# Kernel optimization log

Hardware: AMD Instinct MI355X
Metric: run time of the kernel (lower is better)

## Reference

```python
import jax, jax.numpy as jnp
import numpy as np

B, N, D, K = 32, 4096, 128, 512
NPB = 2048          # unique tail nodes per batch (>= K so topk branch is taken)
M = B * NPB         # total unique tail nodes
E = B * N           # total edges
NUM_ENT = 10000


def setup_inputs() -> dict:
    key = jax.random.key(0)
    ks = jax.random.split(key, 18)
    f = lambda k, s: jax.random.normal(k, s, dtype=jnp.float32)
    inp = {
        "q_head": f(ks[0], (B, D)),
        "q_rel": f(ks[1], (B, D)),
        "q_time": f(ks[2], (B, D)),
        "r_neighbor": f(ks[3], (B, N, D)),
        "t_neighbor": f(ks[4], (B, N, D)),
        "time_neighbor": f(ks[5], (B, N, D)),
        "hidden": f(ks[6], (E, D)),
        "tail_emd": jnp.zeros((M, D), jnp.float32),  # scatter out-buffer
    }
    # tail_index: each edge of batch b scatters into that batch's node slab
    local = jax.random.randint(ks[7], (B, N), 0, NPB)
    inp["tail_index"] = (local + jnp.arange(B)[:, None] * NPB).reshape(E).astype(jnp.int32)
    # tail_nodes: [M,3] = (batch id, tail entity, time)
    batch_col = jnp.repeat(jnp.arange(B), NPB)
    tail_col = jax.random.randint(ks[8], (M,), 0, NUM_ENT)
    time_col = jax.random.randint(ks[9], (M,), 0, 365)
    inp["tail_nodes"] = jnp.stack([batch_col, tail_col, time_col], axis=-1).astype(jnp.int32)
    # linear-layer params (torch nn.Linear-style scaling)
    s3, s1 = 1.0 / np.sqrt(3 * D), 1.0 / np.sqrt(D)
    inp["W_q"] = f(ks[10], (3 * D, D)) * s3
    inp["b_q"] = jnp.zeros((D,), jnp.float32)
    inp["W_a"] = f(ks[11], (3 * D, D)) * s3
    inp["b_a"] = jnp.zeros((D,), jnp.float32)
    inp["W_att"] = f(ks[12], (3 * D, 1)) * s3
    inp["b_att"] = jnp.zeros((1,), jnp.float32)
    inp["W_rule"] = f(ks[13], (D, 1)) * s1
    inp["b_rule"] = jnp.zeros((1,), jnp.float32)
    inp["W_out"] = f(ks[14], (D, D)) * s1
    inp["b_out"] = jnp.zeros((D,), jnp.float32)
    return inp


def reference(q_head, q_rel, q_time, r_neighbor, t_neighbor, time_neighbor,
              hidden, tail_emd, tail_index, tail_nodes,
              W_q, b_q, W_a, b_a, W_att, b_att, W_rule, b_rule, W_out, b_out):
    # act = identity (module default). reduce = 'sum'.
    # raw message per edge: [E, D]
    message = (q_head[:, None, :] + r_neighbor + time_neighbor).reshape(E, D)
    # query / neighbor projections
    query = jnp.concatenate([q_head, q_rel, q_time], axis=-1) @ W_q + b_q      # [B, D]
    neigh = jnp.concatenate([r_neighbor, t_neighbor, time_neighbor], -1) @ W_a + b_a  # [B, N, D]
    q = query[:, None, :]
    qa = jnp.concatenate([q * neigh, q - neigh, q + neigh], axis=-1)           # [B, N, 3D]
    att1 = jax.nn.sigmoid(qa @ W_att + b_att).reshape(E, 1)
    att2 = jax.nn.sigmoid(hidden @ W_rule + b_rule)                            # [E, 1]
    att = (att1 + att2) * 0.5
    msg = att * message
    # scatter-sum aggregation over unique tail nodes
    seg = lambda v: jax.ops.segment_sum(v, tail_index, num_segments=M)
    tail_agg = tail_emd + seg(msg)            # scatter(..., out=tail_emd)
    new_hidden = seg(hidden)                  # [M, D]
    agg_att = seg(att[:, 0])                  # [M]
    # per-batch top-k over aggregated attention (each batch has NPB >= K nodes)
    nodes_batch = tail_nodes[:, 0]
    scores = jnp.where(nodes_batch[None, :] == jnp.arange(B)[:, None],
                       agg_att[None, :], -jnp.inf)                             # [B, M]
    _, idx = jax.lax.top_k(scores, K)                                          # [B, K] global node ids
    new_nodes = jnp.stack([tail_nodes[:, 1][idx], tail_nodes[:, 2][idx]], -1)  # [B, K, 2]
    emd = tail_agg[idx]                                                        # [B, K, D]
    hid = new_hidden[idx]                                                      # [B, K, D]
    out_emd = emd @ W_out + b_out                                              # act=identity
    return new_nodes, out_emd, hid
```

## Files before the change

### kernel.cpp

```cpp
#include <hip/hip_runtime.h>
#include <math.h>

#define B 32
#define N 4096
#define D 128
#define KTOP 512
#define NPB 2048
#define MSEG (B * NPB)
#define E (B * N)
#define MAXC 32
#define K7ROWS 16

__global__ __launch_bounds__(384) void k0_precompute(
    const float* __restrict__ qh, const float* __restrict__ qr,
    const float* __restrict__ qt, const float* __restrict__ Wq,
    const float* __restrict__ bq, const float* __restrict__ Wa,
    const float* __restrict__ ba, const float* __restrict__ Watt,
    const float* __restrict__ batt, float* __restrict__ vf,
    float* __restrict__ c2f, int* __restrict__ counts,
    double* __restrict__ aggd) {
  int b = blockIdx.x;
  int tid = threadIdx.x;
  {
    int t = b * 384 + tid;
    float4 z = make_float4(0.f, 0.f, 0.f, 0.f);
    float4* cz = (float4*)counts;
    float4* az = (float4*)aggd;
    for (int i = t; i < 16384; i += 12288) cz[i] = z;
    for (int i = t; i < 32768; i += 12288) az[i] = z;
  }
  int d = tid & 127;
  int g = tid >> 7;
  __shared__ double part[3][128];
  __shared__ double u[128];
  __shared__ double red[128];
  const float* xs = (g == 0 ? qh : (g == 1 ? qr : qt)) + b * 128;
  const float* Wg = Wq + g * 128 * 128;
  double a0 = 0, a1 = 0, a2 = 0, a3 = 0;
#pragma unroll 4
  for (int i = 0; i < 128; i += 4) {
    a0 += (double)xs[i] * (double)Wg[i * 128 + d];
    a1 += (double)xs[i + 1] * (double)Wg[(i + 1) * 128 + d];
    a2 += (double)xs[i + 2] * (double)Wg[(i + 2) * 128 + d];
    a3 += (double)xs[i + 3] * (double)Wg[(i + 3) * 128 + d];
  }
  part[g][d] = (a0 + a1) + (a2 + a3);
  __syncthreads();
  if (g == 0) {
    double acc = (double)bq[d] + part[0][d] + part[1][d] + part[2][d];
    double w1 = (double)Watt[d], w2 = (double)Watt[128 + d],
           w3 = (double)Watt[256 + d];
    double ud = acc * w1 - w2 + w3;
    u[d] = ud;
    red[d] = acc * (w2 + w3) + (double)ba[d] * ud;
  }
  __syncthreads();
  for (int s = 64; s > 0; s >>= 1) {
    if (tid < s) red[tid] += red[tid + s];
    __syncthreads();
  }
  if (tid == 0) c2f[b] = (float)(red[0] + (double)batt[0]);
  {
    double v0 = 0, v1 = 0, v2 = 0, v3 = 0;
    const float* Wr = Wa + tid * 128;
#pragma unroll 4
    for (int dd = 0; dd < 128; dd += 4) {
      v0 += (double)Wr[dd] * u[dd];
      v1 += (double)Wr[dd + 1] * u[dd + 1];
      v2 += (double)Wr[dd + 2] * u[dd + 2];
      v3 += (double)Wr[dd + 3] * u[dd + 3];
    }
    vf[b * 384 + tid] = (float)((v0 + v1) + (v2 + v3));
  }
}

__global__ __launch_bounds__(256, 8) void k1_att(
    const float* __restrict__ r, const float* __restrict__ t,
    const float* __restrict__ tm, const float* __restrict__ hidden,
    const float* __restrict__ Wrule, const float* __restrict__ brule,
    const float* __restrict__ vf, const float* __restrict__ c2f,
    const int* __restrict__ tidx, float* __restrict__ attw,
    double* __restrict__ aggd, int* __restrict__ counts,
    int* __restrict__ lists) {
  int tid = threadIdx.x;
  int h = tid >> 5;
  int l = tid & 31;
  int base = blockIdx.x * 64;
  int b = base >> 12;
  const float4* vb = (const float4*)(vf + b * 384);
  float4 v0 = vb[l];
  float4 v1 = vb[32 + l];
  float4 v2 = vb[64 + l];
  float4 wr = ((const float4*)Wrule)[l];
  float c2 = c2f[b];
  float br = brule[0];
  int myseg = 0;
  if (l < 8) myseg = tidx[base + l * 8 + h];
  float mya = 0.f;
  unsigned lo = (unsigned)(l * 4);
  float4 ra[2], ta[2], ma[2], ha[2];
  {
    unsigned eo = ((unsigned)(base + h) << 7) + lo;
    ra[0] = *(const float4*)(r + eo);
    ta[0] = *(const float4*)(t + eo);
    ma[0] = *(const float4*)(tm + eo);
    ha[0] = *(const float4*)(hidden + eo);
  }
#pragma unroll
  for (int i = 0; i < 8; ++i) {
    const int cur = i & 1;
    if (i < 7) {
      const int nxt = cur ^ 1;
      unsigned eo = ((unsigned)(base + (i + 1) * 8 + h) << 7) + lo;
      ra[nxt] = *(const float4*)(r + eo);
      ta[nxt] = *(const float4*)(t + eo);
      ma[nxt] = *(const float4*)(tm + eo);
      ha[nxt] = *(const float4*)(hidden + eo);
    }
    float4 A = ra[cur], T = ta[cur], M = ma[cur], H = ha[cur];
    float p1 = A.x * v0.x + A.y * v0.y + A.z * v0.z + A.w * v0.w;
    p1 += T.x * v1.x + T.y * v1.y + T.z * v1.z + T.w * v1.w;
    p1 += M.x * v2.x + M.y * v2.y + M.z * v2.z + M.w * v2.w;
    float p2 = H.x * wr.x + H.y * wr.y + H.z * wr.z + H.w * wr.w;
#pragma unroll
    for (int off = 16; off > 0; off >>= 1) {
      p1 += __shfl_xor(p1, off);
      p2 += __shfl_xor(p2, off);
    }
    if (l == i) {
      float a1 = 1.0f / (1.0f + expf(-(p1 + c2)));
      float a2 = 1.0f / (1.0f + expf(-(p2 + br)));
      mya = 0.5f * (a1 + a2);
    }
  }
  if (l < 8) {
    int e = base + l * 8 + h;
    attw[e] = mya;
    atomicAdd(&aggd[myseg], (double)mya);
    int pos = atomicAdd(&counts[myseg], 1);
    if (pos < MAXC) lists[myseg * MAXC + pos] = e;
  }
}

__global__ __launch_bounds__(256) void k6_topk(
    const double* __restrict__ aggd, const int* __restrict__ tail_nodes,
    float* __restrict__ out_nodes, int* __restrict__ idxw) {
  __shared__ double sv[2048];
  int b = blockIdx.x >> 3;
  int chunk = blockIdx.x & 7;
  int tid = threadIdx.x;
  for (int s = tid; s < 2048; s += 256) sv[s] = aggd[b * 2048 + s];
  __syncthreads();
  int i = chunk * 256 + tid;
  double vi = sv[i];
  int rank = 0;
#pragma unroll 8
  for (int j = 0; j < 2048; ++j) {
    double vj = sv[j];
    rank += (vj > vi) || (vj == vi && j < i);
  }
  if (rank < KTOP) {
    int gm = b * 2048 + i;
    int p = b * KTOP + rank;
    out_nodes[p * 2 + 0] = (float)tail_nodes[gm * 3 + 1];
    out_nodes[p * 2 + 1] = (float)tail_nodes[gm * 3 + 2];
    idxw[p] = gm;
  }
}

__global__ __launch_bounds__(256) void k7_out(
    const float* __restrict__ tail_emd, const float* __restrict__ r,
    const float* __restrict__ tm, const float* __restrict__ hidden,
    const float* __restrict__ qh, const float* __restrict__ attw,
    const int* __restrict__ counts, const int* __restrict__ lists,
    const float* __restrict__ Wout, const float* __restrict__ bout,
    const int* __restrict__ idxw, float* __restrict__ out_emd,
    float* __restrict__ out_hid) {
  __shared__ float es[K7ROWS][128];
  int tid = threadIdx.x;
  int sub = tid >> 7, d = tid & 127;
  int base = blockIdx.x * K7ROWS;
  int mrow[8], crow[8];
#pragma unroll
  for (int jj = 0; jj < 8; ++jj) mrow[jj] = idxw[base + jj * 2 + sub];
#pragma unroll
  for (int jj = 0; jj < 8; ++jj) crow[jj] = counts[mrow[jj]];
  int4 el[8];
#pragma unroll
  for (int jj = 0; jj < 8; ++jj)
    el[jj] = *(const int4*)(lists + (size_t)mrow[jj] * MAXC);
#pragma unroll
  for (int jj = 0; jj < 8; ++jj) {
    int m = mrow[jj];
    int bb = m >> 11;
    int cnt = crow[jj] > MAXC ? MAXC : crow[jj];
    float accT = tail_emd[(size_t)m * 128 + d];
    float accH = 0.f;
    float qhd = qh[bb * 128 + d];
    int e0 = el[jj].x, e1 = el[jj].y, e2 = el[jj].z, e3 = el[jj].w;
    if (cnt > 0) {
      float a = attw[e0];
      size_t eo = (size_t)e0 * 128 + d;
      accT += a * (qhd + r[eo] + tm[eo]);
      accH += hidden[eo];
    }
    if (cnt > 1) {
      float a = attw[e1];
      size_t eo = (size_t)e1 * 128 + d;
      accT += a * (qhd + r[eo] + tm[eo]);
      accH += hidden[eo];
    }
    if (cnt > 2) {
      float a = attw[e2];
      size_t eo = (size_t)e2 * 128 + d;
      accT += a * (qhd + r[eo] + tm[eo]);
      accH += hidden[eo];
    }
    if (cnt > 3) {
      float a = attw[e3];
      size_t eo = (size_t)e3 * 128 + d;
      accT += a * (qhd + r[eo] + tm[eo]);
      accH += hidden[eo];
    }
    for (int k = 4; k < cnt; ++k) {
      int e = lists[(size_t)m * MAXC + k];
      float a = attw[e];
      size_t eo = (size_t)e * 128 + d;
      accT += a * (qhd + r[eo] + tm[eo]);
      accH += hidden[eo];
    }
    es[jj * 2 + sub][d] = accT;
    out_hid[(size_t)(base + jj * 2 + sub) * 128 + d] = accH;
  }
  __syncthreads();
  int cg = tid & 31;
  int rg = tid >> 5;
  float4 bo = *(const float4*)(bout + cg * 4);
  float acc0x = bo.x, acc0y = bo.y, acc0z = bo.z, acc0w = bo.w;
  float acc1x = bo.x, acc1y = bo.y, acc1z = bo.z, acc1w = bo.w;
#pragma unroll 4
  for (int i = 0; i < 128; ++i) {
    float4 w = *(const float4*)(Wout + i * 128 + cg * 4);
    float e0 = es[rg * 2 + 0][i];
    float e1 = es[rg * 2 + 1][i];
    acc0x += e0 * w.x; acc0y += e0 * w.y; acc0z += e0 * w.z; acc0w += e0 * w.w;
    acc1x += e1 * w.x; acc1y += e1 * w.y; acc1z += e1 * w.z; acc1w += e1 * w.w;
  }
  size_t r0 = (size_t)(base + rg * 2) * 128 + cg * 4;
  *(float4*)(out_emd + r0) = make_float4(acc0x, acc0y, acc0z, acc0w);
  *(float4*)(out_emd + r0 + 128) = make_float4(acc1x, acc1y, acc1z, acc1w);
}

extern "C" void kernel_launch(void* const* d_in, const int* in_sizes, int n_in,
                              void* d_out, int out_size, void* d_ws,
                              size_t ws_size, hipStream_t stream) {
  const float* q_head = (const float*)d_in[0];
  const float* q_rel = (const float*)d_in[1];
  const float* q_time = (const float*)d_in[2];
  const float* r_nb = (const float*)d_in[3];
  const float* t_nb = (const float*)d_in[4];
  const float* tm_nb = (const float*)d_in[5];
  const float* hidden = (const float*)d_in[6];
  const float* tail_emd = (const float*)d_in[7];
  const int* tail_index = (const int*)d_in[8];
  const int* tail_nodes = (const int*)d_in[9];
  const float* W_q = (const float*)d_in[10];
  const float* b_q = (const float*)d_in[11];
  const float* W_a = (const float*)d_in[12];
  const float* b_a = (const float*)d_in[13];
  const float* W_att = (const float*)d_in[14];
  const float* b_att = (const float*)d_in[15];
  const float* W_rule = (const float*)d_in[16];
  const float* b_rule = (const float*)d_in[17];
  const float* W_out = (const float*)d_in[18];
  const float* b_out = (const float*)d_in[19];

  char* ws = (char*)d_ws;
  float* vf = (float*)(ws + 0);
  float* c2f = (float*)(ws + 49152);
  float* attw = (float*)(ws + 49280);
  int* counts = (int*)(ws + 573568);
  double* aggd = (double*)(ws + 835712);
  int* lists = (int*)(ws + 1360000);
  int* idxw = (int*)(ws + 9748608);

  float* out_nodes = (float*)d_out;
  float* out_emd = (float*)d_out + (size_t)B * KTOP * 2;
  float* out_hid = out_emd + (size_t)B * KTOP * 128;

  k0_precompute<<<B, 384, 0, stream>>>(q_head, q_rel, q_time, W_q, b_q, W_a,
                                       b_a, W_att, b_att, vf, c2f, counts,
                                       aggd);
  k1_att<<<E / 64, 256, 0, stream>>>(r_nb, t_nb, tm_nb, hidden, W_rule, b_rule,
                                     vf, c2f, tail_index, attw, aggd, counts,
                                     lists);
  k6_topk<<<B * 8, 256, 0, stream>>>(aggd, tail_nodes, out_nodes, idxw);
  k7_out<<<(B * KTOP) / K7ROWS, 256, 0, stream>>>(tail_emd, r_nb, tm_nb,
                                                  hidden, q_head, attw, counts,
                                                  lists, W_out, b_out, idxw,
                                                  out_emd, out_hid);
}
```

Measured before the change: 431.7 us.

## Store edge lists as 16-bit local ids, batch gather loads, halve k1 grid

Edge lists per segment now hold 16-bit batch-local edge ids instead of 32-bit global ids. This halves list storage and the first-entry load in the output kernel, which moves from an int4 to a uint2. The first four gathers in k7 are issued unconditionally and masked by multiplication rather than branches, so the loads can be in flight at the same time. k1 now processes two 64-edge chunks per block with half the grid, cutting per-block setup. The unconditional loads read garbage list slots when the count is below four. They stay in bounds only because the ids are masked into the batch range, and a garbage attw value that is NaN or Inf times a zero mask would give NaN.

```diff
diff --git a/kernel.cpp b/kernel.cpp
--- a/kernel.cpp
+++ b/kernel.cpp
@@ -81,12 +81,12 @@
     const float* __restrict__ vf, const float* __restrict__ c2f,
     const int* __restrict__ tidx, float* __restrict__ attw,
     double* __restrict__ aggd, int* __restrict__ counts,
-    int* __restrict__ lists) {
+    unsigned short* __restrict__ lists) {
   int tid = threadIdx.x;
   int h = tid >> 5;
   int l = tid & 31;
-  int base = blockIdx.x * 64;
-  int b = base >> 12;
+  int blk = blockIdx.x;
+  int b = blk >> 5;
   const float4* vb = (const float4*)(vf + b * 384);
   float4 v0 = vb[l];
   float4 v1 = vb[32 + l];
@@ -94,51 +94,55 @@
   float4 wr = ((const float4*)Wrule)[l];
   float c2 = c2f[b];
   float br = brule[0];
-  int myseg = 0;
-  if (l < 8) myseg = tidx[base + l * 8 + h];
-  float mya = 0.f;
   unsigned lo = (unsigned)(l * 4);
-  float4 ra[2], ta[2], ma[2], ha[2];
-  {
-    unsigned eo = ((unsigned)(base + h) << 7) + lo;
-    ra[0] = *(const float4*)(r + eo);
-    ta[0] = *(const float4*)(t + eo);
-    ma[0] = *(const float4*)(tm + eo);
-    ha[0] = *(const float4*)(hidden + eo);
-  }
-#pragma unroll
-  for (int i = 0; i < 8; ++i) {
-    const int cur = i & 1;
-    if (i < 7) {
-      const int nxt = cur ^ 1;
-      unsigned eo = ((unsigned)(base + (i + 1) * 8 + h) << 7) + lo;
-      ra[nxt] = *(const float4*)(r + eo);
-      ta[nxt] = *(const float4*)(t + eo);
-      ma[nxt] = *(const float4*)(tm + eo);
-      ha[nxt] = *(const float4*)(hidden + eo);
-    }
-    float4 A = ra[cur], T = ta[cur], M = ma[cur], H = ha[cur];
-    float p1 = A.x * v0.x + A.y * v0.y + A.z * v0.z + A.w * v0.w;
-    p1 += T.x * v1.x + T.y * v1.y + T.z * v1.z + T.w * v1.w;
-    p1 += M.x * v2.x + M.y * v2.y + M.z * v2.z + M.w * v2.w;
-    float p2 = H.x * wr.x + H.y * wr.y + H.z * wr.z + H.w * wr.w;
-#pragma unroll
-    for (int off = 16; off > 0; off >>= 1) {
-      p1 += __shfl_xor(p1, off);
-      p2 += __shfl_xor(p2, off);
-    }
-    if (l == i) {
-      float a1 = 1.0f / (1.0f + expf(-(p1 + c2)));
-      float a2 = 1.0f / (1.0f + expf(-(p2 + br)));
-      mya = 0.5f * (a1 + a2);
-    }
-  }
-  if (l < 8) {
-    int e = base + l * 8 + h;
-    attw[e] = mya;
-    atomicAdd(&aggd[myseg], (double)mya);
-    int pos = atomicAdd(&counts[myseg], 1);
-    if (pos < MAXC) lists[myseg * MAXC + pos] = e;
+  for (int pass = 0; pass < 2; ++pass) {
+    int base = blk * 128 + pass * 64;
+    int myseg = 0;
+    if (l < 8) myseg = tidx[base + l * 8 + h];
+    float mya = 0.f;
+    float4 ra[2], ta[2], ma[2], ha[2];
+    {
+      unsigned eo = ((unsigned)(base + h) << 7) + lo;
+      ra[0] = *(const float4*)(r + eo);
+      ta[0] = *(const float4*)(t + eo);
+      ma[0] = *(const float4*)(tm + eo);
+      ha[0] = *(const float4*)(hidden + eo);
+    }
+#pragma unroll
+    for (int i = 0; i < 8; ++i) {
+      const int cur = i & 1;
+      if (i < 7) {
+        const int nxt = cur ^ 1;
+        unsigned eo = ((unsigned)(base + (i + 1) * 8 + h) << 7) + lo;
+        ra[nxt] = *(const float4*)(r + eo);
+        ta[nxt] = *(const float4*)(t + eo);
+        ma[nxt] = *(const float4*)(tm + eo);
+        ha[nxt] = *(const float4*)(hidden + eo);
+      }
+      float4 A = ra[cur], T = ta[cur], M = ma[cur], H = ha[cur];
+      float p1 = A.x * v0.x + A.y * v0.y + A.z * v0.z + A.w * v0.w;
+      p1 += T.x * v1.x + T.y * v1.y + T.z * v1.z + T.w * v1.w;
+      p1 += M.x * v2.x + M.y * v2.y + M.z * v2.z + M.w * v2.w;
+      float p2 = H.x * wr.x + H.y * wr.y + H.z * wr.z + H.w * wr.w;
+#pragma unroll
+      for (int off = 16; off > 0; off >>= 1) {
+        p1 += __shfl_xor(p1, off);
+        p2 += __shfl_xor(p2, off);
+      }
+      if (l == i) {
+        float a1 = 1.0f / (1.0f + expf(-(p1 + c2)));
+        float a2 = 1.0f / (1.0f + expf(-(p2 + br)));
+        mya = 0.5f * (a1 + a2);
+      }
+    }
+    if (l < 8) {
+      int e = base + l * 8 + h;
+      attw[e] = mya;
+      atomicAdd(&aggd[myseg], (double)mya);
+      int pos = atomicAdd(&counts[myseg], 1);
+      if (pos < MAXC)
+        lists[(unsigned)myseg * MAXC + pos] = (unsigned short)(e & 4095);
+    }
   }
 }
 
@@ -172,7 +176,7 @@
     const float* __restrict__ tail_emd, const float* __restrict__ r,
     const float* __restrict__ tm, const float* __restrict__ hidden,
     const float* __restrict__ qh, const float* __restrict__ attw,
-    const int* __restrict__ counts, const int* __restrict__ lists,
+    const int* __restrict__ counts, const unsigned short* __restrict__ lists,
     const float* __restrict__ Wout, const float* __restrict__ bout,
     const int* __restrict__ idxw, float* __restrict__ out_emd,
     float* __restrict__ out_hid) {
@@ -185,47 +189,42 @@
   for (int jj = 0; jj < 8; ++jj) mrow[jj] = idxw[base + jj * 2 + sub];
 #pragma unroll
   for (int jj = 0; jj < 8; ++jj) crow[jj] = counts[mrow[jj]];
-  int4 el[8];
+  uint2 el[8];
 #pragma unroll
   for (int jj = 0; jj < 8; ++jj)
-    el[jj] = *(const int4*)(lists + (size_t)mrow[jj] * MAXC);
+    el[jj] = *(const uint2*)(lists + (size_t)mrow[jj] * MAXC);
 #pragma unroll
   for (int jj = 0; jj < 8; ++jj) {
     int m = mrow[jj];
     int bb = m >> 11;
+    unsigned ebase = (unsigned)bb << 12;
     int cnt = crow[jj] > MAXC ? MAXC : crow[jj];
     float accT = tail_emd[(size_t)m * 128 + d];
     float accH = 0.f;
     float qhd = qh[bb * 128 + d];
-    int e0 = el[jj].x, e1 = el[jj].y, e2 = el[jj].z, e3 = el[jj].w;
-    if (cnt > 0) {
-      float a = attw[e0];
-      size_t eo = (size_t)e0 * 128 + d;
-      accT += a * (qhd + r[eo] + tm[eo]);
-      accH += hidden[eo];
-    }
-    if (cnt > 1) {
-      float a = attw[e1];
-      size_t eo = (size_t)e1 * 128 + d;
-      accT += a * (qhd + r[eo] + tm[eo]);
-      accH += hidden[eo];
-    }
-    if (cnt > 2) {
-      float a = attw[e2];
-      size_t eo = (size_t)e2 * 128 + d;
-      accT += a * (qhd + r[eo] + tm[eo]);
-      accH += hidden[eo];
-    }
-    if (cnt > 3) {
-      float a = attw[e3];
-      size_t eo = (size_t)e3 * 128 + d;
-      accT += a * (qhd + r[eo] + tm[eo]);
-      accH += hidden[eo];
-    }
+    unsigned e0 = ebase | (el[jj].x & 0xFFFFu);
+    unsigned e1 = ebase | (el[jj].x >> 16);
+    unsigned e2 = ebase | (el[jj].y & 0xFFFFu);
+    unsigned e3 = ebase | (el[jj].y >> 16);
+    float m0 = cnt > 0 ? 1.f : 0.f;
+    float m1 = cnt > 1 ? 1.f : 0.f;
+    float m2 = cnt > 2 ? 1.f : 0.f;
+    float m3 = cnt > 3 ? 1.f : 0.f;
+    float a0 = attw[e0], a1 = attw[e1], a2 = attw[e2], a3 = attw[e3];
+    unsigned o0 = (e0 << 7) + d, o1 = (e1 << 7) + d;
+    unsigned o2 = (e2 << 7) + d, o3 = (e3 << 7) + d;
+    float r0 = r[o0], r1 = r[o1], r2 = r[o2], r3 = r[o3];
+    float t0 = tm[o0], t1 = tm[o1], t2 = tm[o2], t3 = tm[o3];
+    float h0 = hidden[o0], h1 = hidden[o1], h2 = hidden[o2], h3 = hidden[o3];
+    accT += m0 * a0 * (qhd + r0 + t0);
+    accT += m1 * a1 * (qhd + r1 + t1);
+    accT += m2 * a2 * (qhd + r2 + t2);
+    accT += m3 * a3 * (qhd + r3 + t3);
+    accH += m0 * h0 + m1 * h1 + m2 * h2 + m3 * h3;
     for (int k = 4; k < cnt; ++k) {
-      int e = lists[(size_t)m * MAXC + k];
+      unsigned e = ebase | lists[(size_t)m * MAXC + k];
       float a = attw[e];
-      size_t eo = (size_t)e * 128 + d;
+      unsigned eo = (e << 7) + d;
       accT += a * (qhd + r[eo] + tm[eo]);
       accH += hidden[eo];
     }
@@ -246,9 +245,9 @@
     acc0x += e0 * w.x; acc0y += e0 * w.y; acc0z += e0 * w.z; acc0w += e0 * w.w;
     acc1x += e1 * w.x; acc1y += e1 * w.y; acc1z += e1 * w.z; acc1w += e1 * w.w;
   }
-  size_t r0 = (size_t)(base + rg * 2) * 128 + cg * 4;
-  *(float4*)(out_emd + r0) = make_float4(acc0x, acc0y, acc0z, acc0w);
-  *(float4*)(out_emd + r0 + 128) = make_float4(acc1x, acc1y, acc1z, acc1w);
+  size_t r0o = (size_t)(base + rg * 2) * 128 + cg * 4;
+  *(float4*)(out_emd + r0o) = make_float4(acc0x, acc0y, acc0z, acc0w);
+  *(float4*)(out_emd + r0o + 128) = make_float4(acc1x, acc1y, acc1z, acc1w);
 }
 
 extern "C" void kernel_launch(void* const* d_in, const int* in_sizes, int n_in,
@@ -281,8 +280,8 @@
   float* attw = (float*)(ws + 49280);
   int* counts = (int*)(ws + 573568);
   double* aggd = (double*)(ws + 835712);
-  int* lists = (int*)(ws + 1360000);
-  int* idxw = (int*)(ws + 9748608);
+  unsigned short* lists = (unsigned short*)(ws + 1360000);
+  int* idxw = (int*)(ws + 5554304);
 
   float* out_nodes = (float*)d_out;
   float* out_emd = (float*)d_out + (size_t)B * KTOP * 2;
@@ -291,9 +290,9 @@
   k0_precompute<<<B, 384, 0, stream>>>(q_head, q_rel, q_time, W_q, b_q, W_a,
                                        b_a, W_att, b_att, vf, c2f, counts,
                                        aggd);
-  k1_att<<<E / 64, 256, 0, stream>>>(r_nb, t_nb, tm_nb, hidden, W_rule, b_rule,
-                                     vf, c2f, tail_index, attw, aggd, counts,
-                                     lists);
+  k1_att<<<E / 128, 256, 0, stream>>>(r_nb, t_nb, tm_nb, hidden, W_rule,
+                                      b_rule, vf, c2f, tail_index, attw, aggd,
+                                      counts, lists);
   k6_topk<<<B * 8, 256, 0, stream>>>(aggd, tail_nodes, out_nodes, idxw);
   k7_out<<<(B * KTOP) / K7ROWS, 256, 0, stream>>>(tail_emd, r_nb, tm_nb,
                                                   hidden, q_head, attw, counts,
```

Result: no change. 424.9 us (-1.6%).
